# Kernel optimization log

Hardware: AMD Instinct MI355X
Metric: run time of the kernel (lower is better)

The kernel has to match this reference:

```python
import jax, jax.numpy as jnp
import numpy as np

STRIDE = 2

def setup_inputs() -> dict:
    key = jax.random.key(0)
    k1, k2, k3, k4, k5 = jax.random.split(key, 5)
    B, Cin, H, W = 16, 64, 128, 128
    Cout, kh, kw = 64, 3, 3
    oh = ow = 63  # ceil((H - kh + 1) / STRIDE)
    inp = jax.random.normal(k1, (B, Cin, H, W), dtype=jnp.float32)
    fan_in = Cin * kh * kw
    weight = jax.random.normal(k2, (Cout, Cin, kh, kw), dtype=jnp.float32) / np.sqrt(fan_in)
    bias = jax.random.normal(k3, (Cout,), dtype=jnp.float32) * 0.01
    selh = jax.random.randint(k4, (oh, ow), 0, STRIDE, dtype=jnp.int32)
    selw = jax.random.randint(k5, (oh, ow), 0, STRIDE, dtype=jnp.int32)
    return {"input": inp, "weight": weight, "bias": bias, "selh": selh, "selw": selw}


def reference(input, weight, bias, selh, selw):
    # Stochastic downsampled conv: per output pixel (i,j), pick the patch at
    # row i*stride + selh[i,j], col j*stride + selw[i,j], then apply the conv GEMM.
    Cout, Cin, kh, kw = weight.shape
    oh, ow = selh.shape
    # top-left corner of the selected patch for each output pixel
    rng_h = selh + jnp.arange(0, oh * STRIDE, STRIDE, dtype=jnp.int32)[:, None]   # (oh, ow)
    rng_w = selw + jnp.arange(0, ow * STRIDE, STRIDE, dtype=jnp.int32)[None, :]   # (oh, ow)
    # full patch index grids: (oh, ow, kh, kw)
    ih = rng_h[:, :, None, None] + jnp.arange(kh, dtype=jnp.int32)[None, None, :, None]
    iw = rng_w[:, :, None, None] + jnp.arange(kw, dtype=jnp.int32)[None, None, None, :]
    # gather selected im2col patches only (avoids materializing the full unfold)
    patches = input[:, :, ih, iw]  # (B, Cin, oh, ow, kh, kw)
    out = jnp.einsum('bcyxhw,ochw->boyx', patches, weight) + bias[None, :, None, None]
    return out  # (B, Cout, oh, ow)
```

## Files before the change

kernel.cpp:

```cpp
#include <hip/hip_runtime.h>


#define B_    16
#define CIN   64
#define H_    128
#define W_    128
#define COUT  64
#define OH    63
#define OW    63
#define NPIX  (OH * OW)
#define KTOT  (CIN * 9)

typedef short  short8  __attribute__((ext_vector_type(8)));
typedef float  float4v __attribute__((ext_vector_type(4)));

__device__ inline short f2bf(float f) {
    union { float f; unsigned u; } x; x.f = f;
    unsigned r = x.u + 0x7fffu + ((x.u >> 16) & 1u);
    return (short)(r >> 16);
}

__global__ __launch_bounds__(256)
void repack_bf16(const float* __restrict__ in, const float* __restrict__ wgt,
                 short* __restrict__ nhwc, short* __restrict__ wgt_t) {
    if (blockIdx.y == H_) {
        const int bid = blockIdx.z * 2 + blockIdx.x;
        for (int e = bid * 256 + (int)threadIdx.x; e < COUT * KTOT; e += 32 * 256) {
            const int o   = e / KTOT;
            const int rem = e - o * KTOT;
            const int c   = rem / 9;
            const int tap = rem - c * 9;
            wgt_t[o * KTOT + tap * CIN + c] = f2bf(wgt[e]);
        }
        return;
    }

    __shared__ float T[64 * 65];
    const int tid = threadIdx.x;
    const int w0  = blockIdx.x * 64;
    const int h   = blockIdx.y;
    const int b   = blockIdx.z;

    {
        const int w4 = tid & 15;
        const int cl = tid >> 4;
#pragma unroll
        for (int i = 0; i < 4; ++i) {
            const int c = cl + 16 * i;
            const float4 v = *(const float4*)&in[((b * CIN + c) * H_ + h) * W_ + w0 + 4 * w4];
            T[c * 65 + 4 * w4 + 0] = v.x;
            T[c * 65 + 4 * w4 + 1] = v.y;
            T[c * 65 + 4 * w4 + 2] = v.z;
            T[c * 65 + 4 * w4 + 3] = v.w;
        }
    }
    __syncthreads();
    {
        const int cg = tid & 7;
        const int wl = tid >> 3;
#pragma unroll
        for (int i = 0; i < 2; ++i) {
            const int w = wl + 32 * i;
            short8 v;
#pragma unroll
            for (int t = 0; t < 8; ++t)
                v[t] = f2bf(T[(8 * cg + t) * 65 + w]);
            *(short8*)&nhwc[((b * H_ + h) * W_ + w0 + w) * CIN + 8 * cg] = v;
        }
    }
}

#define PIXT  16
#define BT    4
#define LDO   65

__global__ __launch_bounds__(256, 4)
void sconv2davg_mfma(const short* __restrict__ nhwc,
                     const short* __restrict__ wgt_t,
                     const float* __restrict__ bias,
                     const int* __restrict__ selh,
                     const int* __restrict__ selw,
                     float* __restrict__ out) {
    __shared__ __align__(16) float Ot[64 * LDO];

    const int tid = threadIdx.x;
    const int p0  = blockIdx.x * PIXT;
    const int b0  = blockIdx.y * BT;

    const int ln = tid & 15;
    const int hl = (tid >> 4) & 3;
    const int wv = tid >> 6;

    const int m  = 16 * wv + ln;
    const int pl = m >> 2;
    const int bl = m & 3;
    int p = p0 + pl;
    if (p > NPIX - 1) p = NPIX - 1;
    const int y   = p / OW;
    const int x   = p - y * OW;
    const int ih0 = 2 * y + selh[p];
    const int iw0 = 2 * x + selw[p];

    const short* A0 = &nhwc[(((b0 + bl) * H_ + ih0) * W_ + iw0) * CIN + hl * 8];
    const short* A1 = A0 + W_ * CIN;
    const short* A2 = A1 + W_ * CIN;
    const short* Bp = &wgt_t[ln * KTOT + hl * 8];

    float4v acc[4];
#pragma unroll
    for (int j = 0; j < 4; ++j) acc[j] = (float4v){0.f, 0.f, 0.f, 0.f};

#pragma unroll
    for (int cc = 0; cc < 2; ++cc) {
        const int c0 = cc * 32;
#pragma unroll
        for (int tap = 0; tap < 9; ++tap) {
            const int kh = tap / 3;
            const int kw = tap - 3 * kh;
            const short* Ar = (kh == 0) ? A0 : ((kh == 1) ? A1 : A2);
            const short8 a = *(const short8*)&Ar[kw * CIN + c0];
#pragma unroll
            for (int j = 0; j < 4; ++j) {
                const short8 b = *(const short8*)&Bp[(16 * j) * KTOT + tap * CIN + c0];
                acc[j] = __builtin_amdgcn_mfma_f32_16x16x32_bf16(a, b, acc[j], 0, 0, 0);
            }
        }
    }

#pragma unroll
    for (int j = 0; j < 4; ++j) {
        const float bv = bias[16 * j + ln];
#pragma unroll
        for (int r = 0; r < 4; ++r)
            Ot[(16 * wv + 4 * hl + r) * LDO + 16 * j + ln] = acc[j][r] + bv;
    }
    __syncthreads();
    {
        const int pp = tid & 15;
        const int rr = tid >> 4;
        const int p2 = p0 + pp;
        if (p2 < NPIX) {
#pragma unroll
            for (int k = 0; k < 16; ++k) {
                const int rid = k * 16 + rr;
                const int b2  = rid >> 6;
                const int o   = rid & 63;
                out[((b0 + b2) * COUT + o) * NPIX + p2] = Ot[(pp * 4 + b2) * LDO + o];
            }
        }
    }
}

#define FKC   72
#define FLDA  76
__global__ __launch_bounds__(256, 4)
void sconv2davg_fallback(const float* __restrict__ in,
                         const float* __restrict__ wgt,
                         const float* __restrict__ bias,
                         const int* __restrict__ selh,
                         const int* __restrict__ selw,
                         float* __restrict__ out) {
    __shared__ float As[64 * FLDA];
    __shared__ float Ws[64 * FLDA];
    __shared__ int hb_s[4], wb_s[4];
    const int tid = threadIdx.x;
    const int p0  = blockIdx.x * 4;
    if (tid < 4) {
        int p = p0 + tid;
        if (p > NPIX - 1) p = NPIX - 1;
        int y = p / OW;
        int x = p - y * OW;
        hb_s[tid] = 2 * y + selh[p];
        wb_s[tid] = 2 * x + selw[p];
    }
    __syncthreads();
    const int tn = tid & 15, tm = tid >> 4;
    float acc[4][4];
#pragma unroll
    for (int i = 0; i < 4; ++i)
#pragma unroll
        for (int j = 0; j < 4; ++j) acc[i][j] = 0.0f;
    for (int cc = 0; cc < 8; ++cc) {
        const int c0 = cc * 8;
#pragma unroll
        for (int it = 0; it < 18; ++it) {
            int idx = tid + it * 256;
            int m = idx / FKC, rem = idx - m * FKC;
            int cl = rem / 9, r = rem - cl * 9;
            int kh = r / 3, kw = r - kh * 3;
            As[m * FLDA + rem] =
                in[((((m & 15) * CIN) + (c0 + cl)) * H_ + hb_s[m >> 4] + kh) * W_ + wb_s[m >> 4] + kw];
        }
#pragma unroll
        for (int it = 0; it < 18; ++it) {
            int idx = tid + it * 256;
            int o = idx / FKC, kk = idx - o * FKC;
            Ws[o * FLDA + kk] = wgt[o * KTOT + cc * FKC + kk];
        }
        __syncthreads();
#pragma unroll 2
        for (int k0 = 0; k0 < FKC; k0 += 4) {
            float4 a[4], w[4];
#pragma unroll
            for (int i = 0; i < 4; ++i) a[i] = *(const float4*)&As[(4 * tm + i) * FLDA + k0];
#pragma unroll
            for (int j = 0; j < 4; ++j) w[j] = *(const float4*)&Ws[(tn + 16 * j) * FLDA + k0];
#pragma unroll
            for (int i = 0; i < 4; ++i)
#pragma unroll
                for (int j = 0; j < 4; ++j) {
                    acc[i][j] += a[i].x * w[j].x; acc[i][j] += a[i].y * w[j].y;
                    acc[i][j] += a[i].z * w[j].z; acc[i][j] += a[i].w * w[j].w;
                }
        }
        __syncthreads();
    }
    const int p = p0 + (tm >> 2);
    if (p < NPIX) {
#pragma unroll
        for (int i = 0; i < 4; ++i) {
            int b = (tm & 3) * 4 + i;
#pragma unroll
            for (int j = 0; j < 4; ++j)
                out[((b * COUT) + tn + 16 * j) * NPIX + p] = acc[i][j] + bias[tn + 16 * j];
        }
    }
}

extern "C" void kernel_launch(void* const* d_in, const int* in_sizes, int n_in,
                              void* d_out, int out_size, void* d_ws, size_t ws_size,
                              hipStream_t stream) {
    const float* in   = (const float*)d_in[0];
    const float* wgt  = (const float*)d_in[1];
    const float* bias = (const float*)d_in[2];
    const int*   selh = (const int*)d_in[3];
    const int*   selw = (const int*)d_in[4];
    float* out = (float*)d_out;

    const size_t nhwc_elems = (size_t)B_ * H_ * W_ * CIN;
    const size_t need = (nhwc_elems + (size_t)COUT * KTOT) * 2;

    if (ws_size >= need) {
        short* nhwc  = (short*)d_ws;
        short* wgt_t = nhwc + nhwc_elems;
        repack_bf16<<<dim3(W_ / 64, H_ + 1, B_), 256, 0, stream>>>(in, wgt, nhwc, wgt_t);
        const int ptiles = (NPIX + PIXT - 1) / PIXT;
        sconv2davg_mfma<<<dim3(ptiles, B_ / BT), 256, 0, stream>>>(
            nhwc, wgt_t, bias, selh, selw, out);
    } else {
        sconv2davg_fallback<<<(NPIX + 3) / 4, 256, 0, stream>>>(
            in, wgt, bias, selh, selw, out);
    }
}
```

Before: 147.9 us.

## Stage gathered patches in LDS via global_load_lds and split waves over output channels

Each wave now holds the weights for its own 16 output channels in registers, where before every wave loaded all four channel groups. The gathered input patches for all 64 rows (pixel×batch) are staged into shared memory with async global_load_lds, and all waves read them from there. This removes the redundant per-wave weight loads and lets MFMAs read A operands from LDS. In exchange it uses 72KB of LDS per block and lowers the occupancy target to 2 blocks/SM, and it uses a full barrier before any compute, with no overlap.

```diff
diff --git a/kernel.cpp b/kernel.cpp
--- a/kernel.cpp
+++ b/kernel.cpp
@@ -74,14 +74,14 @@
 #define BT    4
 #define LDO   65
 
-__global__ __launch_bounds__(256, 4)
+__global__ __launch_bounds__(256, 2)
 void sconv2davg_mfma(const short* __restrict__ nhwc,
                      const short* __restrict__ wgt_t,
                      const float* __restrict__ bias,
                      const int* __restrict__ selh,
                      const int* __restrict__ selw,
                      float* __restrict__ out) {
-    __shared__ __align__(16) float Ot[64 * LDO];
+    __shared__ __align__(16) short As[18 * 2048];
 
     const int tid = threadIdx.x;
     const int p0  = blockIdx.x * PIXT;
@@ -90,50 +90,63 @@
     const int ln = tid & 15;
     const int hl = (tid >> 4) & 3;
     const int wv = tid >> 6;
-
-    const int m  = 16 * wv + ln;
-    const int pl = m >> 2;
-    const int bl = m & 3;
-    int p = p0 + pl;
-    if (p > NPIX - 1) p = NPIX - 1;
-    const int y   = p / OW;
-    const int x   = p - y * OW;
-    const int ih0 = 2 * y + selh[p];
-    const int iw0 = 2 * x + selw[p];
-
-    const short* A0 = &nhwc[(((b0 + bl) * H_ + ih0) * W_ + iw0) * CIN + hl * 8];
-    const short* A1 = A0 + W_ * CIN;
-    const short* A2 = A1 + W_ * CIN;
-    const short* Bp = &wgt_t[ln * KTOT + hl * 8];
+    const int l  = tid & 63;
+
+    const short* Bp = &wgt_t[(16 * wv + ln) * KTOT + hl * 8];
+    short8 Bv[18];
+#pragma unroll
+    for (int u = 0; u < 18; ++u) {
+        const int cc = u / 9, tap = u - 9 * (u / 9);
+        Bv[u] = *(const short8*)&Bp[tap * CIN + cc * 32];
+    }
+
+    {
+        const int mst = 16 * wv + (l >> 2);
+        const int pl  = mst >> 2;
+        const int bl  = mst & 3;
+        int p = p0 + pl;
+        if (p > NPIX - 1) p = NPIX - 1;
+        const int y   = p / OW;
+        const int x   = p - y * OW;
+        const int ih0 = 2 * y + selh[p];
+        const int iw0 = 2 * x + selw[p];
+        const short* src0 =
+            &nhwc[(((b0 + bl) * H_ + ih0) * W_ + iw0) * CIN + (l & 3) * 8];
+        short* dst0 = &As[wv * 512] + l * 8;
+#pragma unroll
+        for (int u = 0; u < 18; ++u) {
+            const int cc = u / 9, tap = u - 9 * (u / 9);
+            const int kh = tap / 3, kw = tap - 3 * (tap / 3);
+            __builtin_amdgcn_global_load_lds(
+                (const __attribute__((address_space(1))) void*)
+                    (src0 + kh * (W_ * CIN) + kw * CIN + cc * 32),
+                (__attribute__((address_space(3))) void*)(dst0 + u * 2048),
+                16, 0, 0);
+        }
+    }
+    __syncthreads();
 
     float4v acc[4];
 #pragma unroll
-    for (int j = 0; j < 4; ++j) acc[j] = (float4v){0.f, 0.f, 0.f, 0.f};
-
-#pragma unroll
-    for (int cc = 0; cc < 2; ++cc) {
-        const int c0 = cc * 32;
-#pragma unroll
-        for (int tap = 0; tap < 9; ++tap) {
-            const int kh = tap / 3;
-            const int kw = tap - 3 * kh;
-            const short* Ar = (kh == 0) ? A0 : ((kh == 1) ? A1 : A2);
-            const short8 a = *(const short8*)&Ar[kw * CIN + c0];
-#pragma unroll
-            for (int j = 0; j < 4; ++j) {
-                const short8 b = *(const short8*)&Bp[(16 * j) * KTOT + tap * CIN + c0];
-                acc[j] = __builtin_amdgcn_mfma_f32_16x16x32_bf16(a, b, acc[j], 0, 0, 0);
-            }
-        }
-    }
-
-#pragma unroll
-    for (int j = 0; j < 4; ++j) {
-        const float bv = bias[16 * j + ln];
+    for (int i = 0; i < 4; ++i) acc[i] = (float4v){0.f, 0.f, 0.f, 0.f};
+#pragma unroll
+    for (int u = 0; u < 18; ++u) {
+#pragma unroll
+        for (int i = 0; i < 4; ++i) {
+            const short8 a = *(const short8*)
+                &As[u * 2048 + (16 * i + ln) * 32 + hl * 8];
+            acc[i] = __builtin_amdgcn_mfma_f32_16x16x32_bf16(a, Bv[u], acc[i], 0, 0, 0);
+        }
+    }
+    __syncthreads();
+
+    float* Ot = (float*)As;
+    const float bv = bias[16 * wv + ln];
+#pragma unroll
+    for (int i = 0; i < 4; ++i)
 #pragma unroll
         for (int r = 0; r < 4; ++r)
-            Ot[(16 * wv + 4 * hl + r) * LDO + 16 * j + ln] = acc[j][r] + bv;
-    }
+            Ot[(16 * i + 4 * hl + r) * LDO + 16 * wv + ln] = acc[i][r] + bv;
     __syncthreads();
     {
         const int pp = tid & 15;
```

Result: faster. 126.2 us (-14.7%).
